# Kernel optimization log

Measured on AMD Instinct MI355X. Metric: run time of the kernel, lower is better.

## Reference

```python
import jax, jax.numpy as jnp
import numpy as np

N_NODES = 50000
N_EDGES = 800000
IN_CH = 128
HID = 64
OUT_CH = 10
N_LAYERS = 5
N_GRAPHS = 128
BN_EPS = 1e-5


def setup_inputs() -> dict:
    key = jax.random.key(0)
    ks = jax.random.split(key, 20)
    s = 0.1
    inp = {}
    inp["x"] = jax.random.normal(ks[0], (N_NODES, IN_CH), jnp.float32)
    inp["edge_index"] = jax.random.randint(ks[1], (2, N_EDGES), 0, N_NODES, dtype=jnp.int32)
    inp["batch"] = jnp.sort(jax.random.randint(ks[2], (N_NODES,), 0, N_GRAPHS, dtype=jnp.int32))
    # GINConv MLPs: layer 0 maps IN_CH->HID->HID, layers 1..4 map HID->HID->HID
    inp["w1_0"] = jax.random.normal(ks[3], (IN_CH, HID), jnp.float32) * s
    inp["b1_0"] = jnp.zeros((HID,), jnp.float32)
    inp["w2_0"] = jax.random.normal(ks[4], (HID, HID), jnp.float32) * s
    inp["b2_0"] = jnp.zeros((HID,), jnp.float32)
    inp["w1_rest"] = jax.random.normal(ks[5], (N_LAYERS - 1, HID, HID), jnp.float32) * s
    inp["b1_rest"] = jnp.zeros((N_LAYERS - 1, HID), jnp.float32)
    inp["w2_rest"] = jax.random.normal(ks[6], (N_LAYERS - 1, HID, HID), jnp.float32) * s
    inp["b2_rest"] = jnp.zeros((N_LAYERS - 1, HID), jnp.float32)
    # JK 'cat' projection: Linear(N_LAYERS*HID -> HID)
    inp["jk_w"] = jax.random.normal(ks[7], (N_LAYERS * HID, HID), jnp.float32) * s
    inp["jk_b"] = jnp.zeros((HID,), jnp.float32)
    # classifier MLP([HID, HID, OUT]) with batch_norm between
    inp["clf_w1"] = jax.random.normal(ks[8], (HID, HID), jnp.float32) * s
    inp["clf_b1"] = jnp.zeros((HID,), jnp.float32)
    inp["bn_gamma"] = jnp.ones((HID,), jnp.float32)
    inp["bn_beta"] = jnp.zeros((HID,), jnp.float32)
    inp["clf_w2"] = jax.random.normal(ks[9], (HID, OUT_CH), jnp.float32) * s
    inp["clf_b2"] = jnp.zeros((OUT_CH,), jnp.float32)
    return inp


def reference(x, edge_index, batch, w1_0, b1_0, w2_0, b2_0,
              w1_rest, b1_rest, w2_rest, b2_rest, jk_w, jk_b,
              clf_w1, clf_b1, bn_gamma, bn_beta, clf_w2, clf_b2):
    src, dst = edge_index[0], edge_index[1]
    xs = []
    h = x
    for i in range(N_LAYERS):
        # GINConv: mlp((1+eps)*x + sum_{j in N(i)} x_j), eps=0
        agg = jax.ops.segment_sum(h[src], dst, num_segments=N_NODES)  # [N, d]
        z = agg + h
        if i == 0:
            w1, b1, w2, b2 = w1_0, b1_0, w2_0, b2_0
        else:
            w1, b1, w2, b2 = w1_rest[i - 1], b1_rest[i - 1], w2_rest[i - 1], b2_rest[i - 1]
        h = jax.nn.relu(z @ w1 + b1) @ w2 + b2
        # BasicGNN post-conv activation (dropout disabled in inference)
        h = jax.nn.relu(h)
        xs.append(h)
    # JumpingKnowledge 'cat' + projection back to HID
    h = jnp.concatenate(xs, axis=-1) @ jk_w + jk_b  # [N, HID]
    # global_add_pool: per-graph sum
    g = jax.ops.segment_sum(h, batch, num_segments=N_GRAPHS)  # [G, HID]
    # classifier MLP with batch_norm (batch statistics)
    t = g @ clf_w1 + clf_b1
    mu = t.mean(axis=0)
    var = ((t - mu) ** 2).mean(axis=0)
    t = (t - mu) * jax.lax.rsqrt(var + BN_EPS) * bn_gamma + bn_beta
    t = jax.nn.relu(t)
    return t @ clf_w2 + clf_b2  # [G, OUT]
```

## Files before the change

### kernel.cpp

```cpp
#include <hip/hip_runtime.h>
#include <hip/hip_fp16.h>

#define NN 50000
#define NE 800000
#define NG 128
#define OUTC 10
#define SCAN_NB ((NN + 255) / 256)
#define NTILE 3125
#define NODES_PER_PART 6250
#define FILL_CH 6250

__global__ void count_kernel(const int* __restrict__ dst, int* __restrict__ cnt) {
  for (int e = blockIdx.x * blockDim.x + threadIdx.x; e < NE; e += gridDim.x * blockDim.x)
    atomicAdd(&cnt[dst[e]], 1);
}

__global__ __launch_bounds__(256) void partial_kernel(const int* __restrict__ cnt,
                                                      int* __restrict__ part) {
  __shared__ int red[256];
  const int t = threadIdx.x;
  const int idx = blockIdx.x * 256 + t;
  red[t] = (idx < NN) ? cnt[idx] : 0;
  __syncthreads();
#pragma unroll
  for (int off = 128; off > 0; off >>= 1) {
    if (t < off) red[t] += red[t + off];
    __syncthreads();
  }
  if (t == 0) part[blockIdx.x] = red[0];
}

__global__ __launch_bounds__(256) void scanpart_kernel(int* __restrict__ part) {
  __shared__ int s[256];
  const int t = threadIdx.x;
  s[t] = (t < SCAN_NB) ? part[t] : 0;
  __syncthreads();
#pragma unroll
  for (int off = 1; off < 256; off <<= 1) {
    const int v = (t >= off) ? s[t - off] : 0;
    __syncthreads();
    s[t] += v;
    __syncthreads();
  }
  if (t < SCAN_NB) part[t] = (t == 0) ? 0 : s[t - 1];
}

__global__ __launch_bounds__(256) void scatter_scan_kernel(const int* __restrict__ cnt,
                                                           const int* __restrict__ part,
                                                           int* __restrict__ rowptr,
                                                           int* __restrict__ cursor) {
  __shared__ int s[256];
  const int t = threadIdx.x;
  const int idx = blockIdx.x * 256 + t;
  s[t] = (idx < NN) ? cnt[idx] : 0;
  __syncthreads();
#pragma unroll
  for (int off = 1; off < 256; off <<= 1) {
    const int v = (t >= off) ? s[t - off] : 0;
    __syncthreads();
    s[t] += v;
    __syncthreads();
  }
  const int excl = part[blockIdx.x] + ((t == 0) ? 0 : s[t - 1]);
  if (idx < NN) { rowptr[idx] = excl; cursor[idx] = excl; }
  if (idx == 0) rowptr[NN] = NE;
}

__global__ __launch_bounds__(256) void fill_kernel(const int* __restrict__ src,
                                                   const int* __restrict__ dst,
                                                   int* __restrict__ cursor,
                                                   int* __restrict__ esrc) {
  const int p = blockIdx.x & 7;
  const int q = blockIdx.x >> 3;
  const int lo = p * NODES_PER_PART, hi = lo + NODES_PER_PART;
  const int e0 = q * FILL_CH, e1 = e0 + FILL_CH;
  for (int e = e0 + threadIdx.x; e < e1; e += 256) {
    const int d = dst[e];
    if (d >= lo && d < hi) {
      const int pos = atomicAdd(&cursor[d], 1);
      esrc[pos] = src[e];
    }
  }
}

__global__ __launch_bounds__(128) void gbounds_kernel(const int* __restrict__ batch,
                                                      float* __restrict__ gcnt) {
  __shared__ int sb[NG + 1];
  const int g = threadIdx.x;
  int lo = 0, hi = NN;
  while (lo < hi) {
    const int mid = (lo + hi) >> 1;
    if (batch[mid] < g) lo = mid + 1; else hi = mid;
  }
  sb[g] = lo;
  if (g == 0) sb[NG] = NN;
  __syncthreads();
  gcnt[g] = (float)(sb[g + 1] - sb[g]);
}

__global__ __launch_bounds__(256) void proj_kernel(const float* __restrict__ x,
                                                   const float* __restrict__ w1,
                                                   __half* __restrict__ y) {
  __shared__ float sW[128 * 64];
  __shared__ float sX[64 * 128];
  const int t = threadIdx.x, c = t & 63, rg = t >> 6;
  for (int i = t; i < 128 * 64; i += 256) sW[i] = w1[i];
  const int ntiles = (NN + 63) / 64;
  for (int tile = blockIdx.x; tile < ntiles; tile += gridDim.x) {
    const int r0 = tile * 64, nv = min(64, NN - r0);
    __syncthreads();
    for (int i = t; i < nv * 32; i += 256)
      ((float4*)sX)[i] = ((const float4*)(x + (size_t)r0 * 128))[i];
    __syncthreads();
    float acc[16];
#pragma unroll
    for (int i = 0; i < 16; ++i) acc[i] = 0.f;
    for (int k = 0; k < 128; k += 4) {
      const float w0 = sW[(k + 0) * 64 + c], w1v = sW[(k + 1) * 64 + c],
                  w2v = sW[(k + 2) * 64 + c], w3v = sW[(k + 3) * 64 + c];
#pragma unroll
      for (int i = 0; i < 16; ++i) {
        const float4 xv = *(const float4*)&sX[(rg * 16 + i) * 128 + k];
        acc[i] = fmaf(xv.x, w0, acc[i]);
        acc[i] = fmaf(xv.y, w1v, acc[i]);
        acc[i] = fmaf(xv.z, w2v, acc[i]);
        acc[i] = fmaf(xv.w, w3v, acc[i]);
      }
    }
#pragma unroll
    for (int i = 0; i < 16; ++i) {
      const int r = rg * 16 + i;
      if (r < nv) y[(size_t)(r0 + r) * 64 + c] = __float2half(acc[i]);
    }
  }
}

template <bool HASW1, bool WRITEH>
__global__ __launch_bounds__(256) void gin_fused_kernel(
    const __half* __restrict__ hin, const int* __restrict__ rowptr,
    const int* __restrict__ esrc,
    const float* __restrict__ w1, const float* __restrict__ b1,
    const float* __restrict__ w2, const float* __restrict__ b2,
    __half* __restrict__ hout, const int* __restrict__ batch,
    float* __restrict__ gl) {
  __shared__ float sS[4][16 * 64];
  const int t = threadIdx.x, c = t & 63, wv = t >> 6;
  const int wg = blockIdx.x * 4 + wv;
  if (wg >= NTILE) return;
  float* slice = &sS[wv][0];
  const int n0 = wg * 16;
  const int oct = c >> 3, i = c & 7;

  const int rA = n0 + 2 * oct;
  const int pA0 = rowptr[rA], pA1 = rowptr[rA + 1], pB1 = rowptr[rA + 2];
  union H8 { float4 f; __half2 h2[4]; };
  const __half* hch = hin + i * 8;
  float zA[8], zB[8];
  {
    H8 u0, u1;
    u0.f = *(const float4*)(hch + (size_t)rA * 64);
    u1.f = *(const float4*)(hch + (size_t)(rA + 1) * 64);
#pragma unroll
    for (int k = 0; k < 4; ++k) {
      const float2 f0 = __half22float2(u0.h2[k]);
      const float2 f1 = __half22float2(u1.h2[k]);
      zA[2 * k] = f0.x; zA[2 * k + 1] = f0.y;
      zB[2 * k] = f1.x; zB[2 * k + 1] = f1.y;
    }
  }
  int eA = pA0, eB = pA1;
  while (eA + 1 < pA1 && eB + 1 < pB1) {
    const int sA0 = esrc[eA], sA1 = esrc[eA + 1];
    const int sB0 = esrc[eB], sB1 = esrc[eB + 1];
    H8 a0, a1, b0, b1v;
    a0.f = *(const float4*)(hch + (size_t)sA0 * 64);
    a1.f = *(const float4*)(hch + (size_t)sA1 * 64);
    b0.f = *(const float4*)(hch + (size_t)sB0 * 64);
    b1v.f = *(const float4*)(hch + (size_t)sB1 * 64);
#pragma unroll
    for (int k = 0; k < 4; ++k) {
      const float2 fa0 = __half22float2(a0.h2[k]);
      const float2 fa1 = __half22float2(a1.h2[k]);
      const float2 fb0 = __half22float2(b0.h2[k]);
      const float2 fb1 = __half22float2(b1v.h2[k]);
      zA[2 * k]     += fa0.x + fa1.x;
      zA[2 * k + 1] += fa0.y + fa1.y;
      zB[2 * k]     += fb0.x + fb1.x;
      zB[2 * k + 1] += fb0.y + fb1.y;
    }
    eA += 2; eB += 2;
  }
  for (; eA + 1 < pA1; eA += 2) {
    const int s0 = esrc[eA], s1 = esrc[eA + 1];
    H8 u0, u1;
    u0.f = *(const float4*)(hch + (size_t)s0 * 64);
    u1.f = *(const float4*)(hch + (size_t)s1 * 64);
#pragma unroll
    for (int k = 0; k < 4; ++k) {
      const float2 f0 = __half22float2(u0.h2[k]);
      const float2 f1 = __half22float2(u1.h2[k]);
      zA[2 * k]     += f0.x + f1.x;
      zA[2 * k + 1] += f0.y + f1.y;
    }
  }
  if (eA < pA1) {
    H8 u0; u0.f = *(const float4*)(hch + (size_t)esrc[eA] * 64);
#pragma unroll
    for (int k = 0; k < 4; ++k) {
      const float2 f0 = __half22float2(u0.h2[k]);
      zA[2 * k] += f0.x; zA[2 * k + 1] += f0.y;
    }
  }
  for (; eB + 1 < pB1; eB += 2) {
    const int s0 = esrc[eB], s1 = esrc[eB + 1];
    H8 u0, u1;
    u0.f = *(const float4*)(hch + (size_t)s0 * 64);
    u1.f = *(const float4*)(hch + (size_t)s1 * 64);
#pragma unroll
    for (int k = 0; k < 4; ++k) {
      const float2 f0 = __half22float2(u0.h2[k]);
      const float2 f1 = __half22float2(u1.h2[k]);
      zB[2 * k]     += f0.x + f1.x;
      zB[2 * k + 1] += f0.y + f1.y;
    }
  }
  if (eB < pB1) {
    H8 u0; u0.f = *(const float4*)(hch + (size_t)esrc[eB] * 64);
#pragma unroll
    for (int k = 0; k < 4; ++k) {
      const float2 f0 = __half22float2(u0.h2[k]);
      zB[2 * k] += f0.x; zB[2 * k + 1] += f0.y;
    }
  }
  if (!HASW1) {
    const float4 blo = *(const float4*)(b1 + i * 8);
    const float4 bhi = *(const float4*)(b1 + i * 8 + 4);
    zA[0] = fmaxf(zA[0] + blo.x, 0.f); zA[1] = fmaxf(zA[1] + blo.y, 0.f);
    zA[2] = fmaxf(zA[2] + blo.z, 0.f); zA[3] = fmaxf(zA[3] + blo.w, 0.f);
    zA[4] = fmaxf(zA[4] + bhi.x, 0.f); zA[5] = fmaxf(zA[5] + bhi.y, 0.f);
    zA[6] = fmaxf(zA[6] + bhi.z, 0.f); zA[7] = fmaxf(zA[7] + bhi.w, 0.f);
    zB[0] = fmaxf(zB[0] + blo.x, 0.f); zB[1] = fmaxf(zB[1] + blo.y, 0.f);
    zB[2] = fmaxf(zB[2] + blo.z, 0.f); zB[3] = fmaxf(zB[3] + blo.w, 0.f);
    zB[4] = fmaxf(zB[4] + bhi.x, 0.f); zB[5] = fmaxf(zB[5] + bhi.y, 0.f);
    zB[6] = fmaxf(zB[6] + bhi.z, 0.f); zB[7] = fmaxf(zB[7] + bhi.w, 0.f);
  }
  {
    const float4 a0 = {zA[0], zA[1], zA[2], zA[3]};
    const float4 a1 = {zA[4], zA[5], zA[6], zA[7]};
    const float4 b0v = {zB[0], zB[1], zB[2], zB[3]};
    const float4 b1v_ = {zB[4], zB[5], zB[6], zB[7]};
    *(float4*)&slice[(2 * oct) * 64 + i * 8] = a0;
    *(float4*)&slice[(2 * oct) * 64 + i * 8 + 4] = a1;
    *(float4*)&slice[(2 * oct + 1) * 64 + i * 8] = b0v;
    *(float4*)&slice[(2 * oct + 1) * 64 + i * 8 + 4] = b1v_;
  }

  const float b1c = b1[c], b2c = b2[c];
  if (HASW1) {
    float acc[16];
#pragma unroll
    for (int r = 0; r < 16; ++r) acc[r] = b1c;
    for (int kc = 0; kc < 4; ++kc) {
      float wr[16];
#pragma unroll
      for (int j = 0; j < 16; ++j) wr[j] = w1[(kc * 16 + j) * 64 + c];
#pragma unroll
      for (int r = 0; r < 16; ++r) {
        const float* zp = &slice[r * 64 + kc * 16];
        const float4 za = *(const float4*)(zp + 0);
        const float4 zb = *(const float4*)(zp + 4);
        const float4 zc = *(const float4*)(zp + 8);
        const float4 zd = *(const float4*)(zp + 12);
        float a = acc[r];
        a = fmaf(za.x, wr[0], a);  a = fmaf(za.y, wr[1], a);
        a = fmaf(za.z, wr[2], a);  a = fmaf(za.w, wr[3], a);
        a = fmaf(zb.x, wr[4], a);  a = fmaf(zb.y, wr[5], a);
        a = fmaf(zb.z, wr[6], a);  a = fmaf(zb.w, wr[7], a);
        a = fmaf(zc.x, wr[8], a);  a = fmaf(zc.y, wr[9], a);
        a = fmaf(zc.z, wr[10], a); a = fmaf(zc.w, wr[11], a);
        a = fmaf(zd.x, wr[12], a); a = fmaf(zd.y, wr[13], a);
        a = fmaf(zd.z, wr[14], a); a = fmaf(zd.w, wr[15], a);
        acc[r] = a;
      }
    }
#pragma unroll
    for (int r = 0; r < 16; ++r) slice[r * 64 + c] = fmaxf(acc[r], 0.f);
  }

  float acc2[16];
#pragma unroll
  for (int r = 0; r < 16; ++r) acc2[r] = b2c;
  for (int kc = 0; kc < 4; ++kc) {
    float wr[16];
#pragma unroll
    for (int j = 0; j < 16; ++j) wr[j] = w2[(kc * 16 + j) * 64 + c];
#pragma unroll
    for (int r = 0; r < 16; ++r) {
      const float* hp = &slice[r * 64 + kc * 16];
      const float4 za = *(const float4*)(hp + 0);
      const float4 zb = *(const float4*)(hp + 4);
      const float4 zc = *(const float4*)(hp + 8);
      const float4 zd = *(const float4*)(hp + 12);
      float a = acc2[r];
      a = fmaf(za.x, wr[0], a);  a = fmaf(za.y, wr[1], a);
      a = fmaf(za.z, wr[2], a);  a = fmaf(za.w, wr[3], a);
      a = fmaf(zb.x, wr[4], a);  a = fmaf(zb.y, wr[5], a);
      a = fmaf(zb.z, wr[6], a);  a = fmaf(zb.w, wr[7], a);
      a = fmaf(zc.x, wr[8], a);  a = fmaf(zc.y, wr[9], a);
      a = fmaf(zc.z, wr[10], a); a = fmaf(zc.w, wr[11], a);
      a = fmaf(zd.x, wr[12], a); a = fmaf(zd.y, wr[13], a);
      a = fmaf(zd.z, wr[14], a); a = fmaf(zd.w, wr[15], a);
      acc2[r] = a;
    }
  }
  float pacc = 0.f;
  int cur = batch[n0];
#pragma unroll
  for (int r = 0; r < 16; ++r) {
    const float hval = fmaxf(acc2[r], 0.f);
    if (WRITEH) hout[(size_t)(n0 + r) * 64 + c] = __float2half(hval);
    const int b = batch[n0 + r];
    if (b != cur) {
      atomicAdd(&gl[(size_t)cur * 64 + c], pacc);
      pacc = 0.f;
      cur = b;
    }
    pacc += hval;
  }
  atomicAdd(&gl[(size_t)cur * 64 + c], pacc);
}

__global__ __launch_bounds__(64) void jk_fold_kernel(
    const float* __restrict__ g5, const float* __restrict__ gcnt,
    const float* __restrict__ jkw, const float* __restrict__ jkb,
    const float* __restrict__ w1, const float* __restrict__ b1,
    float* __restrict__ tmat) {
  __shared__ float sg[64];
  const int gi = blockIdx.x, c = threadIdx.x;
  float a = jkb[c] * gcnt[gi];
  for (int l = 0; l < 5; ++l) {
    const float* gv = &g5[(size_t)(l * NG + gi) * 64];
    const float* wv = &jkw[(size_t)l * 64 * 64];
#pragma unroll 8
    for (int k = 0; k < 64; ++k) a = fmaf(gv[k], wv[k * 64 + c], a);
  }
  sg[c] = a;
  __syncthreads();
  float tv = b1[c];
#pragma unroll 8
  for (int k = 0; k < 64; ++k) tv = fmaf(sg[k], w1[k * 64 + c], tv);
  tmat[gi * 64 + c] = tv;
}

__global__ __launch_bounds__(256) void bn_out_kernel(
    const float* __restrict__ tmat, const float* __restrict__ gamma,
    const float* __restrict__ beta, const float* __restrict__ w2,
    const float* __restrict__ b2, float* __restrict__ out) {
  __shared__ float sT[NG * 64];
  __shared__ float sW2[64 * OUTC];
  __shared__ float sMu[64], sRs[64];
  const int t = threadIdx.x;
  for (int i = t; i < NG * 64; i += 256) sT[i] = tmat[i];
  for (int i = t; i < 64 * OUTC; i += 256) sW2[i] = w2[i];
  __syncthreads();
  if (t < 64) {
    float s = 0.f;
    for (int gi = 0; gi < NG; ++gi) s += sT[gi * 64 + t];
    const float mu = s / NG;
    float v = 0.f;
    for (int gi = 0; gi < NG; ++gi) { const float d = sT[gi * 64 + t] - mu; v += d * d; }
    v /= NG;
    sMu[t] = mu;
    sRs[t] = rsqrtf(v + 1e-5f);
  }
  __syncthreads();
  for (int idx = t; idx < NG * 64; idx += 256) {
    const int cc = idx & 63;
    sT[idx] = fmaxf((sT[idx] - sMu[cc]) * sRs[cc] * gamma[cc] + beta[cc], 0.f);
  }
  __syncthreads();
  for (int idx = t; idx < NG * OUTC; idx += 256) {
    const int gi = idx / OUTC, o = idx % OUTC;
    float a = b2[o];
    for (int k = 0; k < 64; ++k) a = fmaf(sT[gi * 64 + k], sW2[k * OUTC + o], a);
    out[idx] = a;
  }
}

extern "C" void kernel_launch(void* const* d_in, const int* in_sizes, int n_in,
                              void* d_out, int out_size, void* d_ws, size_t ws_size,
                              hipStream_t stream) {
  const float* x     = (const float*)d_in[0];
  const int*   ei    = (const int*)d_in[1];
  const int*   batch = (const int*)d_in[2];
  const float* w1_0  = (const float*)d_in[3];
  const float* b1_0  = (const float*)d_in[4];
  const float* w2_0  = (const float*)d_in[5];
  const float* b2_0  = (const float*)d_in[6];
  const float* w1_r  = (const float*)d_in[7];
  const float* b1_r  = (const float*)d_in[8];
  const float* w2_r  = (const float*)d_in[9];
  const float* b2_r  = (const float*)d_in[10];
  const float* jk_w  = (const float*)d_in[11];
  const float* jk_b  = (const float*)d_in[12];
  const float* cw1   = (const float*)d_in[13];
  const float* cb1   = (const float*)d_in[14];
  const float* bng   = (const float*)d_in[15];
  const float* bnb   = (const float*)d_in[16];
  const float* cw2   = (const float*)d_in[17];
  const float* cb2   = (const float*)d_in[18];
  float* out = (float*)d_out;

  char* base = (char*)d_ws;
  size_t o = 0;
  auto take = [&](size_t n) { char* p = base + o; o = (o + n + 255) & ~(size_t)255; return p; };
  int*    cnt    = (int*)take((size_t)NN * 4);
  int*    rowptr = (int*)take((size_t)(NN + 1) * 4);
  int*    cursor = (int*)take((size_t)NN * 4);
  int*    part   = (int*)take((size_t)SCAN_NB * 4);
  int*    esrc   = (int*)take((size_t)NE * 4);
  __half* hA     = (__half*)take((size_t)NN * 64 * 2);
  __half* hB     = (__half*)take((size_t)NN * 64 * 2);
  float*  g5     = (float*)take((size_t)5 * NG * 64 * 4);
  float*  gcnt   = (float*)take((size_t)NG * 4);
  float*  tmat   = (float*)take((size_t)NG * 64 * 4);
  (void)ws_size; (void)in_sizes; (void)n_in; (void)out_size;

  hipMemsetAsync(cnt, 0, (size_t)NN * 4, stream);
  hipMemsetAsync(g5, 0, (size_t)5 * NG * 64 * 4, stream);

  const int* src = ei;
  const int* dst = ei + NE;
  count_kernel<<<1024, 256, 0, stream>>>(dst, cnt);
  partial_kernel<<<SCAN_NB, 256, 0, stream>>>(cnt, part);
  scanpart_kernel<<<1, 256, 0, stream>>>(part);
  scatter_scan_kernel<<<SCAN_NB, 256, 0, stream>>>(cnt, part, rowptr, cursor);
  fill_kernel<<<1024, 256, 0, stream>>>(src, dst, cursor, esrc);
  gbounds_kernel<<<1, 128, 0, stream>>>(batch, gcnt);

  const int GRID = (NTILE + 3) / 4;

  proj_kernel<<<512, 256, 0, stream>>>(x, w1_0, hB);
  gin_fused_kernel<false, true><<<GRID, 256, 0, stream>>>(
      hB, rowptr, esrc, nullptr, b1_0, w2_0, b2_0, hA, batch, g5);
  const __half* hin = hA;
  __half* hout = hB;
  for (int l = 1; l < 5; ++l) {
    if (l < 4) {
      gin_fused_kernel<true, true><<<GRID, 256, 0, stream>>>(
          hin, rowptr, esrc, w1_r + (size_t)(l - 1) * 64 * 64,
          b1_r + (size_t)(l - 1) * 64, w2_r + (size_t)(l - 1) * 64 * 64,
          b2_r + (size_t)(l - 1) * 64, hout, batch, g5 + (size_t)l * NG * 64);
    } else {
      gin_fused_kernel<true, false><<<GRID, 256, 0, stream>>>(
          hin, rowptr, esrc, w1_r + (size_t)(l - 1) * 64 * 64,
          b1_r + (size_t)(l - 1) * 64, w2_r + (size_t)(l - 1) * 64 * 64,
          b2_r + (size_t)(l - 1) * 64, hout, batch, g5 + (size_t)l * NG * 64);
    }
    __half* tmp = (__half*)hin;
    hin = hout;
    hout = tmp;
  }

  jk_fold_kernel<<<NG, 64, 0, stream>>>(g5, gcnt, jk_w, jk_b, cw1, cb1, tmat);
  bn_out_kernel<<<1, 256, 0, stream>>>(tmat, bng, bnb, cw2, cb2, out);
}
```

Before: 395.3 us.

## Cut preprocessing launches and accumulate neighbor sums in packed half2

Several independent changes. The separate scan-of-partials kernel is merged into scatter_scan, where every block redundantly scans the partial sums, and the graph-bounds kernel is folded into jk_fold as a per-block binary search. Both remove small launches. count_kernel now reads int4 and issues four atomics per thread. The GIN aggregation accumulates neighbor features with packed __hadd2 in fp16 instead of converting each value to fp32, which saves conversion ALU work but loses precision on sums over high-degree nodes.

New measurement: 390.9 us. Within noise of the previous version (-1.1%).

```diff
diff --git a/kernel.cpp b/kernel.cpp
--- a/kernel.cpp
+++ b/kernel.cpp
@@ -11,8 +11,14 @@
 #define FILL_CH 6250
 
 __global__ void count_kernel(const int* __restrict__ dst, int* __restrict__ cnt) {
-  for (int e = blockIdx.x * blockDim.x + threadIdx.x; e < NE; e += gridDim.x * blockDim.x)
-    atomicAdd(&cnt[dst[e]], 1);
+  const int idx = blockIdx.x * blockDim.x + threadIdx.x;
+  if (idx < NE / 4) {
+    const int4 d = ((const int4*)dst)[idx];
+    atomicAdd(&cnt[d.x], 1);
+    atomicAdd(&cnt[d.y], 1);
+    atomicAdd(&cnt[d.z], 1);
+    atomicAdd(&cnt[d.w], 1);
+  }
 }
 
 __global__ __launch_bounds__(256) void partial_kernel(const int* __restrict__ cnt,
@@ -30,38 +36,28 @@
   if (t == 0) part[blockIdx.x] = red[0];
 }
 
-__global__ __launch_bounds__(256) void scanpart_kernel(int* __restrict__ part) {
-  __shared__ int s[256];
-  const int t = threadIdx.x;
-  s[t] = (t < SCAN_NB) ? part[t] : 0;
-  __syncthreads();
-#pragma unroll
-  for (int off = 1; off < 256; off <<= 1) {
-    const int v = (t >= off) ? s[t - off] : 0;
-    __syncthreads();
-    s[t] += v;
-    __syncthreads();
-  }
-  if (t < SCAN_NB) part[t] = (t == 0) ? 0 : s[t - 1];
-}
-
 __global__ __launch_bounds__(256) void scatter_scan_kernel(const int* __restrict__ cnt,
                                                            const int* __restrict__ part,
                                                            int* __restrict__ rowptr,
                                                            int* __restrict__ cursor) {
   __shared__ int s[256];
+  __shared__ int sp[256];
   const int t = threadIdx.x;
+  sp[t] = (t < SCAN_NB) ? part[t] : 0;
   const int idx = blockIdx.x * 256 + t;
   s[t] = (idx < NN) ? cnt[idx] : 0;
   __syncthreads();
 #pragma unroll
   for (int off = 1; off < 256; off <<= 1) {
     const int v = (t >= off) ? s[t - off] : 0;
+    const int vp = (t >= off) ? sp[t - off] : 0;
     __syncthreads();
     s[t] += v;
+    sp[t] += vp;
     __syncthreads();
   }
-  const int excl = part[blockIdx.x] + ((t == 0) ? 0 : s[t - 1]);
+  const int pbase = (blockIdx.x == 0) ? 0 : sp[blockIdx.x - 1];
+  const int excl = pbase + ((t == 0) ? 0 : s[t - 1]);
   if (idx < NN) { rowptr[idx] = excl; cursor[idx] = excl; }
   if (idx == 0) rowptr[NN] = NE;
 }
@@ -81,21 +77,6 @@
       esrc[pos] = src[e];
     }
   }
-}
-
-__global__ __launch_bounds__(128) void gbounds_kernel(const int* __restrict__ batch,
-                                                      float* __restrict__ gcnt) {
-  __shared__ int sb[NG + 1];
-  const int g = threadIdx.x;
-  int lo = 0, hi = NN;
-  while (lo < hi) {
-    const int mid = (lo + hi) >> 1;
-    if (batch[mid] < g) lo = mid + 1; else hi = mid;
-  }
-  sb[g] = lo;
-  if (g == 0) sb[NG] = NN;
-  __syncthreads();
-  gcnt[g] = (float)(sb[g + 1] - sb[g]);
 }
 
 __global__ __launch_bounds__(256) void proj_kernel(const float* __restrict__ x,
@@ -155,18 +136,13 @@
   const int pA0 = rowptr[rA], pA1 = rowptr[rA + 1], pB1 = rowptr[rA + 2];
   union H8 { float4 f; __half2 h2[4]; };
   const __half* hch = hin + i * 8;
-  float zA[8], zB[8];
+  __half2 zA2[4], zB2[4];
   {
     H8 u0, u1;
     u0.f = *(const float4*)(hch + (size_t)rA * 64);
     u1.f = *(const float4*)(hch + (size_t)(rA + 1) * 64);
 #pragma unroll
-    for (int k = 0; k < 4; ++k) {
-      const float2 f0 = __half22float2(u0.h2[k]);
-      const float2 f1 = __half22float2(u1.h2[k]);
-      zA[2 * k] = f0.x; zA[2 * k + 1] = f0.y;
-      zB[2 * k] = f1.x; zB[2 * k + 1] = f1.y;
-    }
+    for (int k = 0; k < 4; ++k) { zA2[k] = u0.h2[k]; zB2[k] = u1.h2[k]; }
   }
   int eA = pA0, eB = pA1;
   while (eA + 1 < pA1 && eB + 1 < pB1) {
@@ -179,14 +155,8 @@
     b1v.f = *(const float4*)(hch + (size_t)sB1 * 64);
 #pragma unroll
     for (int k = 0; k < 4; ++k) {
-      const float2 fa0 = __half22float2(a0.h2[k]);
-      const float2 fa1 = __half22float2(a1.h2[k]);
-      const float2 fb0 = __half22float2(b0.h2[k]);
-      const float2 fb1 = __half22float2(b1v.h2[k]);
-      zA[2 * k]     += fa0.x + fa1.x;
-      zA[2 * k + 1] += fa0.y + fa1.y;
-      zB[2 * k]     += fb0.x + fb1.x;
-      zB[2 * k + 1] += fb0.y + fb1.y;
+      zA2[k] = __hadd2(zA2[k], __hadd2(a0.h2[k], a1.h2[k]));
+      zB2[k] = __hadd2(zB2[k], __hadd2(b0.h2[k], b1v.h2[k]));
     }
     eA += 2; eB += 2;
   }
@@ -196,20 +166,12 @@
     u0.f = *(const float4*)(hch + (size_t)s0 * 64);
     u1.f = *(const float4*)(hch + (size_t)s1 * 64);
 #pragma unroll
-    for (int k = 0; k < 4; ++k) {
-      const float2 f0 = __half22float2(u0.h2[k]);
-      const float2 f1 = __half22float2(u1.h2[k]);
-      zA[2 * k]     += f0.x + f1.x;
-      zA[2 * k + 1] += f0.y + f1.y;
-    }
+    for (int k = 0; k < 4; ++k) zA2[k] = __hadd2(zA2[k], __hadd2(u0.h2[k], u1.h2[k]));
   }
   if (eA < pA1) {
     H8 u0; u0.f = *(const float4*)(hch + (size_t)esrc[eA] * 64);
 #pragma unroll
-    for (int k = 0; k < 4; ++k) {
-      const float2 f0 = __half22float2(u0.h2[k]);
-      zA[2 * k] += f0.x; zA[2 * k + 1] += f0.y;
-    }
+    for (int k = 0; k < 4; ++k) zA2[k] = __hadd2(zA2[k], u0.h2[k]);
   }
   for (; eB + 1 < pB1; eB += 2) {
     const int s0 = esrc[eB], s1 = esrc[eB + 1];
@@ -217,20 +179,20 @@
     u0.f = *(const float4*)(hch + (size_t)s0 * 64);
     u1.f = *(const float4*)(hch + (size_t)s1 * 64);
 #pragma unroll
-    for (int k = 0; k < 4; ++k) {
-      const float2 f0 = __half22float2(u0.h2[k]);
-      const float2 f1 = __half22float2(u1.h2[k]);
-      zB[2 * k]     += f0.x + f1.x;
-      zB[2 * k + 1] += f0.y + f1.y;
-    }
+    for (int k = 0; k < 4; ++k) zB2[k] = __hadd2(zB2[k], __hadd2(u0.h2[k], u1.h2[k]));
   }
   if (eB < pB1) {
     H8 u0; u0.f = *(const float4*)(hch + (size_t)esrc[eB] * 64);
 #pragma unroll
-    for (int k = 0; k < 4; ++k) {
-      const float2 f0 = __half22float2(u0.h2[k]);
-      zB[2 * k] += f0.x; zB[2 * k + 1] += f0.y;
-    }
+    for (int k = 0; k < 4; ++k) zB2[k] = __hadd2(zB2[k], u0.h2[k]);
+  }
+  float zA[8], zB[8];
+#pragma unroll
+  for (int k = 0; k < 4; ++k) {
+    const float2 fa = __half22float2(zA2[k]);
+    const float2 fb = __half22float2(zB2[k]);
+    zA[2 * k] = fa.x; zA[2 * k + 1] = fa.y;
+    zB[2 * k] = fb.x; zB[2 * k + 1] = fb.y;
   }
   if (!HASW1) {
     const float4 blo = *(const float4*)(b1 + i * 8);
@@ -331,13 +293,18 @@
 }
 
 __global__ __launch_bounds__(64) void jk_fold_kernel(
-    const float* __restrict__ g5, const float* __restrict__ gcnt,
+    const float* __restrict__ g5, const int* __restrict__ batch,
     const float* __restrict__ jkw, const float* __restrict__ jkb,
     const float* __restrict__ w1, const float* __restrict__ b1,
     float* __restrict__ tmat) {
   __shared__ float sg[64];
   const int gi = blockIdx.x, c = threadIdx.x;
-  float a = jkb[c] * gcnt[gi];
+  int lo = 0, hi = NN;
+  while (lo < hi) { const int m = (lo + hi) >> 1; if (batch[m] < gi) lo = m + 1; else hi = m; }
+  int lo2 = lo, hi2 = NN;
+  while (lo2 < hi2) { const int m = (lo2 + hi2) >> 1; if (batch[m] < gi + 1) lo2 = m + 1; else hi2 = m; }
+  const float cntg = (float)(lo2 - lo);
+  float a = jkb[c] * cntg;
   for (int l = 0; l < 5; ++l) {
     const float* gv = &g5[(size_t)(l * NG + gi) * 64];
     const float* wv = &jkw[(size_t)l * 64 * 64];
@@ -422,7 +389,6 @@
   __half* hA     = (__half*)take((size_t)NN * 64 * 2);
   __half* hB     = (__half*)take((size_t)NN * 64 * 2);
   float*  g5     = (float*)take((size_t)5 * NG * 64 * 4);
-  float*  gcnt   = (float*)take((size_t)NG * 4);
   float*  tmat   = (float*)take((size_t)NG * 64 * 4);
   (void)ws_size; (void)in_sizes; (void)n_in; (void)out_size;
 
@@ -431,12 +397,10 @@
 
   const int* src = ei;
   const int* dst = ei + NE;
-  count_kernel<<<1024, 256, 0, stream>>>(dst, cnt);
+  count_kernel<<<(NE / 4 + 255) / 256, 256, 0, stream>>>(dst, cnt);
   partial_kernel<<<SCAN_NB, 256, 0, stream>>>(cnt, part);
-  scanpart_kernel<<<1, 256, 0, stream>>>(part);
   scatter_scan_kernel<<<SCAN_NB, 256, 0, stream>>>(cnt, part, rowptr, cursor);
   fill_kernel<<<1024, 256, 0, stream>>>(src, dst, cursor, esrc);
-  gbounds_kernel<<<1, 128, 0, stream>>>(batch, gcnt);
 
   const int GRID = (NTILE + 3) / 4;
 
@@ -462,6 +426,6 @@
     hout = tmp;
   }
 
-  jk_fold_kernel<<<NG, 64, 0, stream>>>(g5, gcnt, jk_w, jk_b, cw1, cb1, tmat);
+  jk_fold_kernel<<<NG, 64, 0, stream>>>(g5, batch, jk_w, jk_b, cw1, cb1, tmat);
   bn_out_kernel<<<1, 256, 0, stream>>>(tmat, bng, bnb, cw2, cb2, out);
 }
```
